# Kernel tuning notes

Hardware: AMD Instinct MI355X
Metric: run time of the kernel (lower is better)

The kernel has to match this reference:

```python
import jax, jax.numpy as jnp
import numpy as np

VAR0, VAR1 = 0.1, 0.2      # cfg['variance'] (standard SSD)
CONF_THRESH = 0.01
TOP_K = 200


def setup_inputs() -> dict:
    key = jax.random.key(0)
    k1, k2, k3 = jax.random.split(key, 3)
    B, P, C = 8, 25575, 81
    return {
        "loc_data": jax.random.normal(k1, (B, P, 4), jnp.float32),
        "conf_data": jax.random.uniform(k2, (B, P, C), jnp.float32),
        "prior_data": jax.random.uniform(k3, (1, P, 4), jnp.float32),
    }


def _decode(loc, priors):
    # SSD box decode: loc [B,P,4], priors [P,4] (cx, cy, w, h)
    centers = priors[..., :2] + loc[..., :2] * VAR0 * priors[..., 2:]
    wh = priors[..., 2:] * jnp.exp(loc[..., 2:] * VAR1)
    mins = centers - wh * 0.5
    return jnp.concatenate([mins, mins + wh], axis=-1)  # [B,P,4] xyxy


def reference(loc_data, conf_data, prior_data):
    priors = prior_data[0]                       # [P,4]
    B, P, C = conf_data.shape
    K = TOP_K
    decoded = _decode(loc_data, priors)          # [B,P,4]
    scores = jnp.transpose(conf_data, (0, 2, 1))  # [B,C,P]
    mask = scores > CONF_THRESH                  # strict gt, as in torch .gt()
    counts = mask.sum(-1)                        # [B,C]

    # --- case B: count > top_k -> keep top_k, sorted descending (torch.topk) ---
    masked = jnp.where(mask, scores, -jnp.inf)
    vals, idx = jax.lax.top_k(masked, K)         # [B,C,K]
    boxes_g = jnp.take_along_axis(decoded[:, None], idx[..., None], axis=2)  # [B,C,K,4]
    valid = vals > CONF_THRESH
    outB = jnp.where(valid[..., None],
                     jnp.concatenate([vals[..., None], boxes_g], axis=-1),
                     0.0)

    # --- case A: count <= top_k -> passing priors in original prior order ---
    entry = jnp.concatenate(
        [scores[..., None], jnp.broadcast_to(decoded[:, None], (B, C, P, 4))], axis=-1)  # [B,C,P,5]
    pos = jnp.where(mask, jnp.cumsum(mask, axis=-1) - 1, K)  # invalid -> dump slot K
    bi = jnp.arange(B)[:, None, None]
    ci = jnp.arange(C)[None, :, None]
    outA = jnp.zeros((B, C, K + 1, 5), scores.dtype).at[bi, ci, pos].set(entry)[:, :, :K]

    return jnp.where((counts <= K)[..., None, None], outA, outB)  # [B,C,K,5]
```

## Files before the change

kernel.cpp:

```cpp
#include <hip/hip_runtime.h>

namespace {

constexpr int B_ = 8;
constexpr int P_ = 25575;
constexpr int C_ = 81;
constexpr int K_ = 200;
constexpr int PC = P_ * C_;
constexpr int EPB = 8192;
constexpr int NB = (PC + EPB - 1) / EPB;
constexpr int NBP = 256;
constexpr int CAPB = 12;
constexpr float CONF_T = 0.01f;
constexpr float PREF = 0.985f;
constexpr float FALLBACK_T = 0.9f;
constexpr int SCAP = 1024;


__global__ __launch_bounds__(256) void scan_k(const float* __restrict__ conf,
                                              int* __restrict__ cntC_g,
                                              int* __restrict__ cntF_g,
                                              unsigned long long* __restrict__ cand) {
  __shared__ int cntC[C_];
  __shared__ int cntF[C_];
  __shared__ unsigned long long list[C_][CAPB];

  const int b = blockIdx.y;
  const int nb = blockIdx.x;
  const int tid = threadIdx.x;
  const int s = nb * EPB;
  const int e = (s + EPB < PC) ? s + EPB : PC;

  for (int i = tid; i < C_; i += 256) { cntC[i] = 0; cntF[i] = 0; }
  __syncthreads();

  const float* cb = conf + (size_t)b * PC;

  auto process = [&](int L, float f) {
    bool isC = (f > PREF);
    bool isF = !(f > CONF_T);
    if (!isC && !isF) return;
    unsigned p = (unsigned)L / 81u;
    unsigned c = (unsigned)L - p * 81u;
    if (isC) {
      int lp = atomicAdd(&cntC[c], 1);
      if (lp < CAPB)
        list[c][lp] = ((unsigned long long)__float_as_uint(f) << 32) |
                      (unsigned long long)(~p);
    } else {
      atomicAdd(&cntF[c], 1);
    }
  };

  const int a0 = s + (b & 3);
  const int n4 = (e - a0) >> 2;
  const int a1 = a0 + (n4 << 2);

  for (int L = s + tid; L < a0; L += 256) process(L, cb[L]);
  const float4* c4 = reinterpret_cast<const float4*>(conf) + (((size_t)b * PC + a0) >> 2);
  for (int k = tid; k < n4; k += 256) {
    float4 q = c4[k];
    float mx = fmaxf(fmaxf(q.x, q.y), fmaxf(q.z, q.w));
    float mn = fminf(fminf(q.x, q.y), fminf(q.z, q.w));
    if ((mx > PREF) || !(mn > CONF_T)) {
      int L = a0 + (k << 2);
      process(L + 0, q.x);
      process(L + 1, q.y);
      process(L + 2, q.z);
      process(L + 3, q.w);
    }
  }
  for (int L = a1 + tid; L < e; L += 256) process(L, cb[L]);

  __syncthreads();
  if (tid < C_) {
    cntC_g[(b * C_ + tid) * NBP + nb] = cntC[tid];
    cntF_g[(b * C_ + tid) * NBP + nb] = cntF[tid];
  }
  for (int idx = tid; idx < C_ * CAPB; idx += 256) {
    int c = idx / CAPB;
    int i = idx - c * CAPB;
    int cc = cntC[c] < CAPB ? cntC[c] : CAPB;
    if (i < cc)
      cand[((size_t)(b * C_ + c) * NB + nb) * CAPB + i] = list[c][i];
  }
}

__global__ __launch_bounds__(512) void select_k(const float* __restrict__ conf,
                                                const float* __restrict__ loc,
                                                const float* __restrict__ prior,
                                                const int* __restrict__ cntC_g,
                                                const int* __restrict__ cntF_g,
                                                const unsigned long long* __restrict__ cand,
                                                float* __restrict__ out) {
  __shared__ unsigned long long skey[SCAP];
  __shared__ float sbox[K_ * 5];
  __shared__ int scnt;
  __shared__ int sFail;
  __shared__ int sflag;

  const int row = blockIdx.x;
  const int b = row / C_;
  const int c = row - b * C_;
  const int tid = threadIdx.x;
  const int BS = 512;

  if (tid == 0) { scnt = 0; sFail = 0; sflag = 0; }
  __syncthreads();

  int myF = 0;
  if (tid < NB) {
    const int cbase = (b * C_ + c) * NBP + tid;
    int cc = cntC_g[cbase];
    myF = cntF_g[cbase];
    if (cc > CAPB) { atomicOr(&sflag, 1); cc = CAPB; }
    if (cc > 0) {
      int pos = atomicAdd(&scnt, cc);
      const unsigned long long* src = cand + ((size_t)(b * C_ + c) * NB + tid) * CAPB;
      for (int i = 0; i < cc; ++i) {
        int q = pos + i;
        if (q < SCAP) skey[q] = src[i];
      }
    }
  }
  for (int o = 32; o; o >>= 1) myF += __shfl_down(myF, o);
  if ((tid & 63) == 0 && myF) atomicAdd(&sFail, myF);
  __syncthreads();

  int n = scnt < SCAP ? scnt : SCAP;
  const int count = P_ - sFail;
  const bool caseA = (count <= K_);
  const bool fb = (!caseA) && (sflag || scnt > SCAP || n < K_);

  if (caseA) {
    if (tid == 0) scnt = 0;
    __syncthreads();
    for (int p = tid; p < P_; p += BS) {
      float f = conf[((size_t)b * P_ + p) * C_ + c];
      if (f > CONF_T) {
        int pos = atomicAdd(&scnt, 1);
        if (pos < SCAP)
          skey[pos] = ((unsigned long long)(~(unsigned)p) << 32) |
                      (unsigned long long)__float_as_uint(f);
      }
    }
    __syncthreads();
    n = scnt < SCAP ? scnt : SCAP;
  } else if (fb) {
    const float thr = (n < K_) ? FALLBACK_T : PREF;
    if (tid == 0) scnt = 0;
    __syncthreads();
    for (int p = tid; p < P_; p += BS) {
      float f = conf[((size_t)b * P_ + p) * C_ + c];
      if (f > thr) {
        int pos = atomicAdd(&scnt, 1);
        if (pos < SCAP)
          skey[pos] = ((unsigned long long)__float_as_uint(f) << 32) |
                      (unsigned long long)(~(unsigned)p);
      }
    }
    __syncthreads();
    n = scnt < SCAP ? scnt : SCAP;
  }

  int m = 2;
  while (m < n) m <<= 1;
  for (int i = n + tid; i < m; i += BS) skey[i] = 0ull;

  for (int kk = 2; kk <= m; kk <<= 1) {
    for (int j = kk >> 1; j > 0; j >>= 1) {
      __syncthreads();
      for (int i = tid; i < m; i += BS) {
        int l = i ^ j;
        if (l > i) {
          unsigned long long a = skey[i], bb = skey[l];
          bool sw = ((i & kk) == 0) ? (a < bb) : (a > bb);
          if (sw) { skey[i] = bb; skey[l] = a; }
        }
      }
    }
  }
  __syncthreads();

  const int n_out = (n < K_) ? n : K_;

  for (int k = tid; k < K_; k += BS) {
    float o0 = 0.f, o1 = 0.f, o2 = 0.f, o3 = 0.f, o4 = 0.f;
    if (k < n_out) {
      unsigned long long key = skey[k];
      unsigned p, vb;
      if (caseA) {
        p = ~(unsigned)(key >> 32);
        vb = (unsigned)key;
      } else {
        vb = (unsigned)(key >> 32);
        p = ~(unsigned)key;
      }
      float4 l4 = reinterpret_cast<const float4*>(loc)[(size_t)b * P_ + p];
      float4 pr = reinterpret_cast<const float4*>(prior)[p];
      float cx = pr.x + l4.x * 0.1f * pr.z;
      float cy = pr.y + l4.y * 0.1f * pr.w;
      float w = pr.z * expf(l4.z * 0.2f);
      float h = pr.w * expf(l4.w * 0.2f);
      float x1 = cx - w * 0.5f;
      float y1 = cy - h * 0.5f;
      o0 = __uint_as_float(vb);
      o1 = x1;
      o2 = y1;
      o3 = x1 + w;
      o4 = y1 + h;
    }
    sbox[k * 5 + 0] = o0;
    sbox[k * 5 + 1] = o1;
    sbox[k * 5 + 2] = o2;
    sbox[k * 5 + 3] = o3;
    sbox[k * 5 + 4] = o4;
  }
  __syncthreads();

  const size_t base = (size_t)row * K_ * 5;
  for (int i = tid; i < K_ * 5; i += BS) out[base + i] = sbox[i];
}

}

extern "C" void kernel_launch(void* const* d_in, const int* in_sizes, int n_in,
                              void* d_out, int out_size, void* d_ws, size_t ws_size,
                              hipStream_t stream) {
  const float* loc = (const float*)d_in[0];
  const float* conf = (const float*)d_in[1];
  const float* prior = (const float*)d_in[2];
  float* out = (float*)d_out;

  int* cntC_g = (int*)d_ws;
  int* cntF_g = cntC_g + B_ * C_ * NBP;
  unsigned long long* cand =
      (unsigned long long*)(cntF_g + B_ * C_ * NBP);

  dim3 grid1(NB, B_);
  scan_k<<<grid1, 256, 0, stream>>>(conf, cntC_g, cntF_g, cand);
  select_k<<<648, 512, 0, stream>>>(conf, loc, prior, cntC_g, cntF_g, cand, out);
}
```

Baseline: 41.99 us.

## Replace bitonic sort with rank-by-counting selection in select kernel

Drops the shared-memory bitonic sort of candidate keys, which needed many barrier-separated passes. Each thread now computes its key's rank by comparing it against all n keys and scatters the decoded box straight to that rank slot. The output buffer is zero-initialised up front so unfilled slots stay zero. The intent is to remove the log^2 sync stages, in exchange for O(n^2) shared-memory reads, which become expensive when n is large (up to 1024).

```diff
diff --git a/kernel.cpp b/kernel.cpp
--- a/kernel.cpp
+++ b/kernel.cpp
@@ -106,6 +106,7 @@
   const int BS = 512;
 
   if (tid == 0) { scnt = 0; sFail = 0; sflag = 0; }
+  for (int i = tid; i < K_ * 5; i += BS) sbox[i] = 0.f;
   __syncthreads();
 
   int myF = 0;
@@ -163,38 +164,18 @@
     n = scnt < SCAP ? scnt : SCAP;
   }
 
-  int m = 2;
-  while (m < n) m <<= 1;
-  for (int i = n + tid; i < m; i += BS) skey[i] = 0ull;
-
-  for (int kk = 2; kk <= m; kk <<= 1) {
-    for (int j = kk >> 1; j > 0; j >>= 1) {
-      __syncthreads();
-      for (int i = tid; i < m; i += BS) {
-        int l = i ^ j;
-        if (l > i) {
-          unsigned long long a = skey[i], bb = skey[l];
-          bool sw = ((i & kk) == 0) ? (a < bb) : (a > bb);
-          if (sw) { skey[i] = bb; skey[l] = a; }
-        }
-      }
-    }
-  }
-  __syncthreads();
-
-  const int n_out = (n < K_) ? n : K_;
-
-  for (int k = tid; k < K_; k += BS) {
-    float o0 = 0.f, o1 = 0.f, o2 = 0.f, o3 = 0.f, o4 = 0.f;
-    if (k < n_out) {
-      unsigned long long key = skey[k];
+  for (int i = tid; i < n; i += BS) {
+    unsigned long long ki = skey[i];
+    int rank = 0;
+    for (int j = 0; j < n; ++j) rank += (skey[j] > ki) ? 1 : 0;
+    if (rank < K_) {
       unsigned p, vb;
       if (caseA) {
-        p = ~(unsigned)(key >> 32);
-        vb = (unsigned)key;
+        p = ~(unsigned)(ki >> 32);
+        vb = (unsigned)ki;
       } else {
-        vb = (unsigned)(key >> 32);
-        p = ~(unsigned)key;
+        vb = (unsigned)(ki >> 32);
+        p = ~(unsigned)ki;
       }
       float4 l4 = reinterpret_cast<const float4*>(loc)[(size_t)b * P_ + p];
       float4 pr = reinterpret_cast<const float4*>(prior)[p];
@@ -204,17 +185,12 @@
       float h = pr.w * expf(l4.w * 0.2f);
       float x1 = cx - w * 0.5f;
       float y1 = cy - h * 0.5f;
-      o0 = __uint_as_float(vb);
-      o1 = x1;
-      o2 = y1;
-      o3 = x1 + w;
-      o4 = y1 + h;
-    }
-    sbox[k * 5 + 0] = o0;
-    sbox[k * 5 + 1] = o1;
-    sbox[k * 5 + 2] = o2;
-    sbox[k * 5 + 3] = o3;
-    sbox[k * 5 + 4] = o4;
+      sbox[rank * 5 + 0] = __uint_as_float(vb);
+      sbox[rank * 5 + 1] = x1;
+      sbox[rank * 5 + 2] = y1;
+      sbox[rank * 5 + 3] = x1 + w;
+      sbox[rank * 5 + 4] = y1 + h;
+    }
   }
   __syncthreads();
 
```

Result: faster. 40.19 us (-4.3%).
